# Optimization experiments

Measured on AMD Instinct MI355X. Metric: run time of the kernel, lower is better.

Reference implementation:

```python
import jax, jax.numpy as jnp
import numpy as np

B, C, L = 8, 256, 4096
OC = C // 2  # out_channels default
EPS = 1e-5


def setup_inputs() -> dict:
    key = jax.random.key(0)
    ks = jax.random.split(key, 12)
    s_in = 1.0 / np.sqrt(C)   # conv1d default init scale (kaiming-uniform-ish)
    s_oc = 1.0 / np.sqrt(OC)
    return {
        "x": jax.random.normal(ks[0], (B, C, L), dtype=jnp.float32),
        "g_w": jax.random.uniform(ks[1], (OC, C), jnp.float32, -s_in, s_in),
        "g_b": jax.random.uniform(ks[2], (OC,), jnp.float32, -s_in, s_in),
        # theta/phi weights: nn.init.normal_(w, 0.02) -> mean 0.02, std 1
        "theta_w": 0.02 + jax.random.normal(ks[3], (OC, C), dtype=jnp.float32),
        "theta_b": jax.random.uniform(ks[4], (OC,), jnp.float32, -s_in, s_in),
        "phi_w": 0.02 + jax.random.normal(ks[5], (OC, C), dtype=jnp.float32),
        "phi_b": jax.random.uniform(ks[6], (OC,), jnp.float32, -s_in, s_in),
        "W_w": jax.random.uniform(ks[7], (C, OC), jnp.float32, -s_oc, s_oc),
        "W_b": jax.random.uniform(ks[8], (C,), jnp.float32, -s_oc, s_oc),
        # BN affine: init to zero in the original; use small random for a meaningful test
        "gamma": 0.1 * jax.random.normal(ks[9], (C,), dtype=jnp.float32),
        "beta": 0.1 * jax.random.normal(ks[10], (C,), dtype=jnp.float32),
    }


def reference(x, g_w, g_b, theta_w, theta_b, phi_w, phi_b, W_w, W_b, gamma, beta):
    # x: (b, c, l). 1x1 conv == per-position linear map over channels.
    g_x = jnp.einsum('oc,bcl->bol', g_w, x) + g_b[None, :, None]        # (b, oc, l)
    theta_x = jnp.einsum('oc,bcl->bol', theta_w, x) + theta_b[None, :, None]
    phi_x = jnp.einsum('oc,bcl->bol', phi_w, x) + phi_b[None, :, None]
    # f = theta^T phi : (b, l, l) quadratic score matrix (no softmax)
    f = jnp.einsum('bok,bom->bkm', theta_x, phi_x)
    N = f.shape[-1]
    # y = (f @ g^T) / N, returned in (b, oc, l) layout
    y = jnp.einsum('bkm,bom->bok', f, g_x) / N
    W_y = jnp.einsum('co,bol->bcl', W_w, y) + W_b[None, :, None]        # (b, c, l)
    # BatchNorm1d (training mode: batch statistics over (b, l), biased var)
    mean = jnp.mean(W_y, axis=(0, 2), keepdims=True)
    var = jnp.mean((W_y - mean) ** 2, axis=(0, 2), keepdims=True)
    W_y = (W_y - mean) * jax.lax.rsqrt(var + EPS)
    W_y = gamma[None, :, None] * W_y + beta[None, :, None]
    return W_y + x  # residual
```

## Files before the change

### kernel.cpp

```cpp
#include <hip/hip_runtime.h>
#include <hip/hip_bf16.h>

#define B_ 8
#define C_ 256
#define OC_ 128
#define L_ 4096
#define EPS_ 1e-5f
#define SPLITK 8

typedef unsigned short u16;
typedef __attribute__((ext_vector_type(4))) unsigned short u16x4;
typedef __attribute__((ext_vector_type(4))) float f32x4;
typedef __attribute__((ext_vector_type(8))) short bf16x8;

__device__ inline u16 f2bf(float f) {
  union { __hip_bfloat16 h; u16 u; } v;
  v.h = __float2bfloat16(f);
  return v.u;
}
__device__ inline float bf2f(u16 u) {
  union { float f; unsigned u; } v;
  v.u = ((unsigned)u) << 16;
  return v.f;
}

__device__ inline void gload_lds16(const void* g, void* lds) {
  __builtin_amdgcn_global_load_lds(
      (const __attribute__((address_space(1))) unsigned int*)g,
      (__attribute__((address_space(3))) unsigned int*)lds, 16, 0, 0);
}

__device__ inline float blockReduceSum(float v, float* red, int nthreads) {
  int tid = threadIdx.x;
  red[tid] = v;
  __syncthreads();
  for (int s = nthreads >> 1; s > 0; s >>= 1) {
    if (tid < s) red[tid] += red[tid + s];
    __syncthreads();
  }
  float r = red[0];
  __syncthreads();
  return r;
}

__global__ __launch_bounds__(256) void k_cvt(const float* __restrict__ x,
                                             u16* __restrict__ Xb,
                                             u16* __restrict__ XbT,
                                             float* __restrict__ spartial) {
  __shared__ u16 T[64][73];
  __shared__ float P[64][17];
  const int b = blockIdx.z, c0 = blockIdx.y * 64, l0 = blockIdx.x * 64;
  const int tid = threadIdx.x;
#pragma unroll
  for (int it = 0; it < 4; ++it) {
    int idx = it * 256 + tid;
    int row = idx >> 4;
    int col = (idx & 15) << 2;
    size_t gi = ((size_t)(b * C_ + c0 + row)) * L_ + l0 + col;
    float4 v = *(const float4*)(x + gi);
    u16 u0 = f2bf(v.x), u1 = f2bf(v.y), u2 = f2bf(v.z), u3 = f2bf(v.w);
    u16x4 u = {u0, u1, u2, u3};
    *(u16x4*)(Xb + gi) = u;
    T[row][col] = u0; T[row][col + 1] = u1; T[row][col + 2] = u2; T[row][col + 3] = u3;
    P[row][idx & 15] = v.x + v.y + v.z + v.w;
  }
  __syncthreads();
  if (tid < 64) {
    float acc = 0.f;
#pragma unroll
    for (int j = 0; j < 16; j++) acc += P[tid][j];
    spartial[(size_t)(b * C_ + c0 + tid) * 64 + blockIdx.x] = acc;
  }
#pragma unroll
  for (int it = 0; it < 4; ++it) {
    int idx = it * 256 + tid;
    int lrow = idx >> 4;
    int ccol = (idx & 15) << 2;
    u16x4 u = {T[ccol][lrow], T[ccol + 1][lrow], T[ccol + 2][lrow], T[ccol + 3][lrow]};
    *(u16x4*)(XbT + ((size_t)b * L_ + l0 + lrow) * C_ + c0 + ccol) = u;
  }
}

__global__ __launch_bounds__(256) void k_xxt(const u16* __restrict__ Xb,
                                             float* __restrict__ Spart) {
  const int b = blockIdx.z, split = blockIdx.y;
  const int ti = blockIdx.x >> 1, tj = blockIdx.x & 1;
  __shared__ u16 lds[2 * 128 * 64];
  const int tid = threadIdx.x, lane = tid & 63;
  const int wid = tid >> 6, wr = wid >> 1, wc = wid & 1;
  const u16* Arows = Xb + ((size_t)b * C_ + ti * 128) * L_;
  const u16* Brows = Xb + ((size_t)b * C_ + tj * 128) * L_;
  const int k0 = split * (L_ / SPLITK);
  f32x4 acc[4][4] = {};
  for (int kt = 0; kt < L_ / SPLITK; kt += 64) {
    __syncthreads();
#pragma unroll
    for (int ch = 0; ch < 4; ch++) {
      int d = ch * 4096 + tid * 16;
      int row = d >> 7;
      int kb = (d & 127) ^ ((row & 7) << 4);
      gload_lds16(Arows + (size_t)row * L_ + k0 + kt + (kb >> 1), (char*)lds + d);
      gload_lds16(Brows + (size_t)row * L_ + k0 + kt + (kb >> 1), (char*)lds + 16384 + d);
    }
    asm volatile("s_waitcnt vmcnt(0)" ::: "memory");
    __syncthreads();
#pragma unroll
    for (int ks = 0; ks < 2; ks++) {
      bf16x8 af[4], bfr[4];
#pragma unroll
      for (int m = 0; m < 4; m++) {
        int row = wr * 64 + m * 16 + (lane & 15);
        int kb = ((ks << 6) + ((lane >> 4) << 4)) ^ ((row & 7) << 4);
        af[m] = *(const bf16x8*)((const char*)lds + row * 128 + kb);
      }
#pragma unroll
      for (int n = 0; n < 4; n++) {
        int row = wc * 64 + n * 16 + (lane & 15);
        int kb = ((ks << 6) + ((lane >> 4) << 4)) ^ ((row & 7) << 4);
        bfr[n] = *(const bf16x8*)((const char*)lds + 16384 + row * 128 + kb);
      }
#pragma unroll
      for (int m = 0; m < 4; m++)
#pragma unroll
        for (int n = 0; n < 4; n++)
          acc[m][n] = __builtin_amdgcn_mfma_f32_16x16x32_bf16(af[m], bfr[n], acc[m][n], 0, 0, 0);
    }
  }
  float* Sp = Spart + ((size_t)split * B_ + b) * C_ * C_;
#pragma unroll
  for (int m = 0; m < 4; m++)
#pragma unroll
    for (int n = 0; n < 4; n++) {
      int r0 = ti * 128 + wr * 64 + m * 16 + ((lane >> 4) << 2);
      int c0 = tj * 128 + wc * 64 + n * 16 + (lane & 15);
#pragma unroll
      for (int r = 0; r < 4; r++)
        Sp[(size_t)(r0 + r) * C_ + c0] = acc[m][n][r];
    }
}

__global__ __launch_bounds__(256) void k_sreduce(const float* __restrict__ Spart,
                                                 const float* __restrict__ spartial,
                                                 const float* __restrict__ g_w,
                                                 float* __restrict__ S,
                                                 float* __restrict__ s,
                                                 float* __restrict__ gwT) {
  const int bid = blockIdx.x, tid = threadIdx.x;
  if (bid < (B_ * C_ * C_) / 256) {
    size_t idx = (size_t)bid * 256 + tid;
    float acc = 0.f;
    for (int sp = 0; sp < SPLITK; sp++) acc += Spart[(size_t)sp * B_ * C_ * C_ + idx];
    S[idx] = acc;
  } else if (bid < (B_ * C_ * C_) / 256 + (B_ * C_) / 256) {
    int idx2 = (bid - (B_ * C_ * C_) / 256) * 256 + tid;
    const float4* sp = (const float4*)(spartial + (size_t)idx2 * 64);
    float acc = 0.f;
#pragma unroll
    for (int i = 0; i < 16; i++) { float4 v = sp[i]; acc += v.x + v.y + v.z + v.w; }
    s[idx2] = acc;
  } else {
    int t = bid - ((B_ * C_ * C_) / 256 + (B_ * C_) / 256);
    int o = t * 8 + (tid & 7);
    int cbase = (tid >> 3) * 8;
#pragma unroll
    for (int k = 0; k < 8; k++) {
      int c = cbase + k;
      gwT[c * OC_ + o] = g_w[o * C_ + c];
    }
  }
}

__global__ __launch_bounds__(256) void k_mid1(const float* __restrict__ S,
                                              const float* __restrict__ s,
                                              const float* __restrict__ phi_w,
                                              const float* __restrict__ phi_b,
                                              const float* __restrict__ gwT,
                                              const float* __restrict__ g_b,
                                              float* __restrict__ MT) {
  const int b = blockIdx.x >> 7, op = blockIdx.x & 127;
  const int tid = threadIdx.x;
  __shared__ float sl[C_], pw[C_], t2[C_], red[256];
  sl[tid] = s[b * C_ + tid];
  pw[tid] = phi_w[op * C_ + tid];
  __syncthreads();
  float ps_op = blockReduceSum(pw[tid] * sl[tid], red, 256);
  float phb = phi_b[op];
  const float* Sb = S + (size_t)b * C_ * C_;
  float t1 = 0.f;
  for (int cp = 0; cp < C_; cp++) t1 += pw[cp] * Sb[(size_t)cp * C_ + tid];
  t2[tid] = t1 + phb * sl[tid];
  __syncthreads();
  const int o = tid & 127, half = tid >> 7;
  float part = 0.f;
  for (int cc = 0; cc < 128; cc++) {
    int cidx = half * 128 + cc;
    part += t2[cidx] * gwT[cidx * OC_ + o];
  }
  red[tid] = part;
  __syncthreads();
  if (tid < OC_) {
    float val = red[tid] + red[tid + 128] + (ps_op + (float)L_ * phb) * g_b[tid];
    MT[((size_t)b * OC_ + tid) * OC_ + op] = val;
  }
}

__global__ __launch_bounds__(128) void k_mid2stats(const float* __restrict__ MT,
                                                   const float* __restrict__ W_w,
                                                   const float* __restrict__ theta_w,
                                                   const float* __restrict__ theta_b,
                                                   const float* __restrict__ W_b,
                                                   const float* __restrict__ S,
                                                   const float* __restrict__ s,
                                                   float* __restrict__ Q,
                                                   float* __restrict__ qv,
                                                   float* __restrict__ sum1,
                                                   float* __restrict__ sum2) {
  const int b = blockIdx.x >> 8, c = blockIdx.x & 255;
  const int tid = threadIdx.x;
  __shared__ float wr_[OC_], U_s[OC_], red[OC_], qrow[C_];
  wr_[tid] = W_w[c * OC_ + tid];
  __syncthreads();
  const float* MTb = MT + (size_t)b * OC_ * OC_;
  float acc = 0.f;
  for (int o = 0; o < OC_; o++) acc += wr_[o] * MTb[(size_t)o * OC_ + tid];
  acc *= (1.0f / (float)L_);
  U_s[tid] = acc;
  float tot = blockReduceSum(acc * theta_b[tid], red, OC_);
  float q_val = tot + W_b[c];
  if (tid == 0) qv[b * C_ + c] = q_val;
  float a2[2];
#pragma unroll
  for (int h = 0; h < 2; h++) {
    int ch = tid + h * OC_;
    float a = 0.f;
    for (int op = 0; op < OC_; op++) a += U_s[op] * theta_w[(size_t)op * C_ + ch];
    a2[h] = a;
    qrow[ch] = a;
    Q[((size_t)b * C_ + c) * C_ + ch] = a;
  }
  __syncthreads();
  const float* Sb = S + (size_t)b * C_ * C_;
  float rq = 0.f, qssum = 0.f;
#pragma unroll
  for (int h = 0; h < 2; h++) {
    int ch = tid + h * OC_;
    float r = 0.f;
    for (int cp = 0; cp < C_; cp++) r += qrow[cp] * Sb[(size_t)cp * C_ + ch];
    rq += r * a2[h];
    qssum += a2[h] * s[b * C_ + ch];
  }
  float e2 = blockReduceSum(rq, red, OC_);
  float qs = blockReduceSum(qssum, red, OC_);
  if (tid == 0) {
    sum1[b * C_ + c] = qs + (float)L_ * q_val;
    sum2[b * C_ + c] = e2 + 2.f * q_val * qs + (float)L_ * q_val * q_val;
  }
}

__global__ __launch_bounds__(256) void k_out(const float* __restrict__ Q,
                                             const float* __restrict__ qv,
                                             const float* __restrict__ sum1,
                                             const float* __restrict__ sum2,
                                             const float* __restrict__ gamma,
                                             const float* __restrict__ beta,
                                             const u16* __restrict__ XbT,
                                             const u16* __restrict__ Xb,
                                             float* __restrict__ out) {
  const int b = blockIdx.z, ct = blockIdx.y, lt = blockIdx.x;
  __shared__ u16 lds[128 * 64];
  __shared__ float gsc_s[128], qp_s[128];
  const int tid = threadIdx.x, lane = tid & 63;
  const int wid = tid >> 6, wr = wid >> 1, wc = wid & 1;
  if (tid < 128) {
    int c = ct * 128 + tid;
    float m = 0.f, e = 0.f;
#pragma unroll
    for (int bb = 0; bb < B_; bb++) {
      m += sum1[bb * C_ + c];
      e += sum2[bb * C_ + c];
    }
    const float inv_n = 1.f / (float)(B_ * L_);
    m *= inv_n;
    e *= inv_n;
    float var = e - m * m;
    float g = gamma[c] * rsqrtf(var + EPS_);
    gsc_s[tid] = g;
    qp_s[tid] = g * (qv[b * C_ + c] - m) + beta[c];
  }
  const u16* Bbase = XbT + ((size_t)b * L_ + lt * 128) * C_;
  const float* Abase = Q + ((size_t)b * C_ + ct * 128) * C_;
  f32x4 acc[4][4] = {};
  for (int k0 = 0; k0 < C_; k0 += 64) {
    __syncthreads();
#pragma unroll
    for (int ch = 0; ch < 4; ch++) {
      int d = ch * 4096 + tid * 16;
      int row = d >> 7;
      int kb = (d & 127) ^ ((row & 7) << 4);
      gload_lds16(Bbase + (size_t)row * C_ + k0 + (kb >> 1), (char*)lds + d);
    }
    asm volatile("s_waitcnt vmcnt(0)" ::: "memory");
    __syncthreads();
#pragma unroll
    for (int ks = 0; ks < 2; ks++) {
      bf16x8 af[4], bfr[4];
#pragma unroll
      for (int m = 0; m < 4; m++) {
        int row = wr * 64 + m * 16 + (lane & 15);
        int kk = k0 + ks * 32 + ((lane >> 4) << 3);
        float g = gsc_s[row];
        const float* src = Abase + (size_t)row * C_ + kk;
        float4 v0 = *(const float4*)src;
        float4 v1 = *(const float4*)(src + 4);
        bf16x8 a;
        a[0] = (short)f2bf(g * v0.x); a[1] = (short)f2bf(g * v0.y);
        a[2] = (short)f2bf(g * v0.z); a[3] = (short)f2bf(g * v0.w);
        a[4] = (short)f2bf(g * v1.x); a[5] = (short)f2bf(g * v1.y);
        a[6] = (short)f2bf(g * v1.z); a[7] = (short)f2bf(g * v1.w);
        af[m] = a;
      }
#pragma unroll
      for (int n = 0; n < 4; n++) {
        int row = wc * 64 + n * 16 + (lane & 15);
        int kb = ((ks << 6) + ((lane >> 4) << 4)) ^ ((row & 7) << 4);
        bfr[n] = *(const bf16x8*)((const char*)lds + row * 128 + kb);
      }
#pragma unroll
      for (int m = 0; m < 4; m++)
#pragma unroll
        for (int n = 0; n < 4; n++)
          acc[m][n] = __builtin_amdgcn_mfma_f32_16x16x32_bf16(af[m], bfr[n], acc[m][n], 0, 0, 0);
    }
  }
#pragma unroll
  for (int m = 0; m < 4; m++)
#pragma unroll
    for (int n = 0; n < 4; n++) {
      int cl = wr * 64 + m * 16 + ((lane >> 4) << 2);
      int c = ct * 128 + cl;
      int l = lt * 128 + wc * 64 + n * 16 + (lane & 15);
#pragma unroll
      for (int r = 0; r < 4; r++) {
        size_t gi = ((size_t)b * C_ + c + r) * L_ + l;
        out[gi] = acc[m][n][r] + bf2f(Xb[gi]) + qp_s[cl + r];
      }
    }
}

extern "C" void kernel_launch(void* const* d_in, const int* in_sizes, int n_in,
                              void* d_out, int out_size, void* d_ws, size_t ws_size,
                              hipStream_t stream) {
  const float* x       = (const float*)d_in[0];
  const float* g_w     = (const float*)d_in[1];
  const float* g_b     = (const float*)d_in[2];
  const float* theta_w = (const float*)d_in[3];
  const float* theta_b = (const float*)d_in[4];
  const float* phi_w   = (const float*)d_in[5];
  const float* phi_b   = (const float*)d_in[6];
  const float* W_w     = (const float*)d_in[7];
  const float* W_b     = (const float*)d_in[8];
  const float* gamma   = (const float*)d_in[9];
  const float* beta    = (const float*)d_in[10];
  float* out = (float*)d_out;

  float* ws = (float*)d_ws;
  size_t off = 0;
  float* Spart    = ws + off; off += (size_t)SPLITK * B_ * C_ * C_;
  float* S        = ws + off; off += (size_t)B_ * C_ * C_;
  float* spartial = ws + off; off += (size_t)B_ * C_ * 64;
  float* s_       = ws + off; off += B_ * C_;
  float* gwT      = ws + off; off += C_ * OC_;
  float* MT       = ws + off; off += (size_t)B_ * OC_ * OC_;
  float* qv       = ws + off; off += B_ * C_;
  float* Q        = ws + off; off += (size_t)B_ * C_ * C_;
  float* sum1     = ws + off; off += B_ * C_;
  float* sum2     = ws + off; off += B_ * C_;
  u16* Xb  = (u16*)(ws + off); off += (size_t)B_ * C_ * L_ / 2;
  u16* XbT = (u16*)(ws + off); off += (size_t)B_ * C_ * L_ / 2;

  k_cvt<<<dim3(L_ / 64, C_ / 64, B_), 256, 0, stream>>>(x, Xb, XbT, spartial);
  k_xxt<<<dim3(4, SPLITK, B_), 256, 0, stream>>>(Xb, Spart);
  k_sreduce<<<(B_ * C_ * C_) / 256 + (B_ * C_) / 256 + 16, 256, 0, stream>>>(
      Spart, spartial, g_w, S, s_, gwT);
  k_mid1<<<B_ * OC_, 256, 0, stream>>>(S, s_, phi_w, phi_b, gwT, g_b, MT);
  k_mid2stats<<<B_ * C_, 128, 0, stream>>>(MT, W_w, theta_w, theta_b, W_b, S, s_,
                                           Q, qv, sum1, sum2);
  k_out<<<dim3(L_ / 128, C_ / 128, B_), 256, 0, stream>>>(Q, qv, sum1, sum2, gamma,
                                                          beta, XbT, Xb, out);
}
```

Before: 118.4 us.

## Register-block small mid kernels to reuse S/MT loads across multiple output rows

The two small matrix-chain kernels (k_mid1, k_mid2stats) now each compute 8 or 16 output rows per block. This reuses every streamed load of S, MT, gwT and theta_w across several accumulators instead of reloading them for each row. Block reductions now use wave shuffles instead of a tree in shared memory with many barriers. The per-column partial sums are stored transposed so the reduction reads coalesced memory. Launching far fewer blocks (128 instead of 1024 or 2048) risks lower GPU occupancy and more register pressure.

```diff
diff --git a/kernel.cpp b/kernel.cpp
--- a/kernel.cpp
+++ b/kernel.cpp
@@ -28,19 +28,6 @@
   __builtin_amdgcn_global_load_lds(
       (const __attribute__((address_space(1))) unsigned int*)g,
       (__attribute__((address_space(3))) unsigned int*)lds, 16, 0, 0);
-}
-
-__device__ inline float blockReduceSum(float v, float* red, int nthreads) {
-  int tid = threadIdx.x;
-  red[tid] = v;
-  __syncthreads();
-  for (int s = nthreads >> 1; s > 0; s >>= 1) {
-    if (tid < s) red[tid] += red[tid + s];
-    __syncthreads();
-  }
-  float r = red[0];
-  __syncthreads();
-  return r;
 }
 
 __global__ __launch_bounds__(256) void k_cvt(const float* __restrict__ x,
@@ -69,7 +56,7 @@
     float acc = 0.f;
 #pragma unroll
     for (int j = 0; j < 16; j++) acc += P[tid][j];
-    spartial[(size_t)(b * C_ + c0 + tid) * 64 + blockIdx.x] = acc;
+    spartial[(size_t)blockIdx.x * (B_ * C_) + b * C_ + c0 + tid] = acc;
   }
 #pragma unroll
   for (int it = 0; it < 4; ++it) {
@@ -153,10 +140,9 @@
     S[idx] = acc;
   } else if (bid < (B_ * C_ * C_) / 256 + (B_ * C_) / 256) {
     int idx2 = (bid - (B_ * C_ * C_) / 256) * 256 + tid;
-    const float4* sp = (const float4*)(spartial + (size_t)idx2 * 64);
     float acc = 0.f;
-#pragma unroll
-    for (int i = 0; i < 16; i++) { float4 v = sp[i]; acc += v.x + v.y + v.z + v.w; }
+#pragma unroll 8
+    for (int i = 0; i < 64; i++) acc += spartial[(size_t)i * (B_ * C_) + idx2];
     s[idx2] = acc;
   } else {
     int t = bid - ((B_ * C_ * C_) / 256 + (B_ * C_) / 256);
@@ -177,83 +163,138 @@
                                               const float* __restrict__ gwT,
                                               const float* __restrict__ g_b,
                                               float* __restrict__ MT) {
-  const int b = blockIdx.x >> 7, op = blockIdx.x & 127;
+  const int b = blockIdx.x >> 4, ot = blockIdx.x & 15;
   const int tid = threadIdx.x;
-  __shared__ float sl[C_], pw[C_], t2[C_], red[256];
+  __shared__ float pw[8][257], t2[8][256], sl[256], ps_s[8], pb_s[8], redw[4][8];
   sl[tid] = s[b * C_ + tid];
-  pw[tid] = phi_w[op * C_ + tid];
-  __syncthreads();
-  float ps_op = blockReduceSum(pw[tid] * sl[tid], red, 256);
-  float phb = phi_b[op];
+#pragma unroll
+  for (int r = 0; r < 8; r++) pw[r][tid] = phi_w[(ot * 8 + r) * C_ + tid];
+  if (tid < 8) pb_s[tid] = phi_b[ot * 8 + tid];
+  __syncthreads();
+  float acc[8] = {};
   const float* Sb = S + (size_t)b * C_ * C_;
-  float t1 = 0.f;
-  for (int cp = 0; cp < C_; cp++) t1 += pw[cp] * Sb[(size_t)cp * C_ + tid];
-  t2[tid] = t1 + phb * sl[tid];
+#pragma unroll 4
+  for (int cp = 0; cp < C_; cp++) {
+    float sv = Sb[(size_t)cp * C_ + tid];
+#pragma unroll
+    for (int r = 0; r < 8; r++) acc[r] += pw[r][cp] * sv;
+  }
+  {
+    const int lane = tid & 63, w = tid >> 6;
+#pragma unroll
+    for (int r = 0; r < 8; r++) {
+      float v = pw[r][tid] * sl[tid];
+#pragma unroll
+      for (int off = 1; off < 64; off <<= 1) v += __shfl_xor(v, off, 64);
+      if (lane == 0) redw[w][r] = v;
+    }
+  }
+#pragma unroll
+  for (int r = 0; r < 8; r++) t2[r][tid] = acc[r] + pb_s[r] * sl[tid];
+  __syncthreads();
+  if (tid < 8) ps_s[tid] = redw[0][tid] + redw[1][tid] + redw[2][tid] + redw[3][tid];
   __syncthreads();
   const int o = tid & 127, half = tid >> 7;
-  float part = 0.f;
-  for (int cc = 0; cc < 128; cc++) {
-    int cidx = half * 128 + cc;
-    part += t2[cidx] * gwT[cidx * OC_ + o];
-  }
-  red[tid] = part;
-  __syncthreads();
-  if (tid < OC_) {
-    float val = red[tid] + red[tid + 128] + (ps_op + (float)L_ * phb) * g_b[tid];
-    MT[((size_t)b * OC_ + tid) * OC_ + op] = val;
-  }
-}
-
-__global__ __launch_bounds__(128) void k_mid2stats(const float* __restrict__ MT,
-                                                   const float* __restrict__ W_w,
-                                                   const float* __restrict__ theta_w,
-                                                   const float* __restrict__ theta_b,
-                                                   const float* __restrict__ W_b,
-                                                   const float* __restrict__ S,
-                                                   const float* __restrict__ s,
-                                                   float* __restrict__ Q,
-                                                   float* __restrict__ qv,
-                                                   float* __restrict__ sum1,
-                                                   float* __restrict__ sum2) {
-  const int b = blockIdx.x >> 8, c = blockIdx.x & 255;
+  float macc[4] = {};
+#pragma unroll 4
+  for (int c = 0; c < C_; c++) {
+    float gv = gwT[c * OC_ + o];
+#pragma unroll
+    for (int rr = 0; rr < 4; rr++) macc[rr] += t2[half * 4 + rr][c] * gv;
+  }
+  float gb = g_b[o];
+#pragma unroll
+  for (int rr = 0; rr < 4; rr++) {
+    int r = half * 4 + rr;
+    int op = ot * 8 + r;
+    MT[((size_t)b * OC_ + o) * OC_ + op] = macc[rr] + (ps_s[r] + (float)L_ * pb_s[r]) * gb;
+  }
+}
+
+__global__ __launch_bounds__(256) void k_mid2(const float* __restrict__ MT,
+                                              const float* __restrict__ W_w,
+                                              const float* __restrict__ theta_w,
+                                              const float* __restrict__ theta_b,
+                                              const float* __restrict__ W_b,
+                                              const float* __restrict__ S,
+                                              const float* __restrict__ s,
+                                              float* __restrict__ Q,
+                                              float* __restrict__ qv,
+                                              float* __restrict__ sum1,
+                                              float* __restrict__ sum2) {
+  const int b = blockIdx.x >> 4, ct = blockIdx.x & 15;
   const int tid = threadIdx.x;
-  __shared__ float wr_[OC_], U_s[OC_], red[OC_], qrow[C_];
-  wr_[tid] = W_w[c * OC_ + tid];
-  __syncthreads();
-  const float* MTb = MT + (size_t)b * OC_ * OC_;
-  float acc = 0.f;
-  for (int o = 0; o < OC_; o++) acc += wr_[o] * MTb[(size_t)o * OC_ + tid];
-  acc *= (1.0f / (float)L_);
-  U_s[tid] = acc;
-  float tot = blockReduceSum(acc * theta_b[tid], red, OC_);
-  float q_val = tot + W_b[c];
-  if (tid == 0) qv[b * C_ + c] = q_val;
-  float a2[2];
-#pragma unroll
-  for (int h = 0; h < 2; h++) {
-    int ch = tid + h * OC_;
+  __shared__ float ww[16][130], u_s[16][130], qtile[16][256];
+  __shared__ float tb[128], s_l[256], q_s[16], redw[2][4][16];
+  s_l[tid] = s[b * C_ + tid];
+  if (tid < 128) tb[tid] = theta_b[tid];
+#pragma unroll
+  for (int rr = 0; rr < 8; rr++) {
+    int idx = rr * 256 + tid;
+    ww[idx >> 7][idx & 127] = W_w[(ct * 16 + (idx >> 7)) * OC_ + (idx & 127)];
+  }
+  __syncthreads();
+  const int op = tid & 127, chalf = tid >> 7;
+  {
+    float uacc[8] = {};
+    const float* MTb = MT + (size_t)b * OC_ * OC_;
+#pragma unroll 4
+    for (int o = 0; o < OC_; o++) {
+      float mv = MTb[(size_t)o * OC_ + op];
+#pragma unroll
+      for (int r = 0; r < 8; r++) uacc[r] += ww[chalf * 8 + r][o] * mv;
+    }
+#pragma unroll
+    for (int r = 0; r < 8; r++) u_s[chalf * 8 + r][op] = uacc[r] * (1.f / (float)L_);
+  }
+  __syncthreads();
+  if (tid < 16) {
     float a = 0.f;
-    for (int op = 0; op < OC_; op++) a += U_s[op] * theta_w[(size_t)op * C_ + ch];
-    a2[h] = a;
-    qrow[ch] = a;
-    Q[((size_t)b * C_ + c) * C_ + ch] = a;
-  }
-  __syncthreads();
+    for (int o2 = 0; o2 < OC_; o2++) a += u_s[tid][o2] * tb[o2];
+    float qval = a + W_b[ct * 16 + tid];
+    q_s[tid] = qval;
+    qv[b * C_ + ct * 16 + tid] = qval;
+  }
+  float qacc[16] = {};
+#pragma unroll 2
+  for (int o = 0; o < OC_; o++) {
+    float tv = theta_w[(size_t)o * C_ + tid];
+#pragma unroll
+    for (int r = 0; r < 16; r++) qacc[r] += u_s[r][o] * tv;
+  }
+#pragma unroll
+  for (int r = 0; r < 16; r++) {
+    qtile[r][tid] = qacc[r];
+    Q[((size_t)b * C_ + ct * 16 + r) * C_ + tid] = qacc[r];
+  }
+  __syncthreads();
+  float yacc[16] = {};
   const float* Sb = S + (size_t)b * C_ * C_;
-  float rq = 0.f, qssum = 0.f;
-#pragma unroll
-  for (int h = 0; h < 2; h++) {
-    int ch = tid + h * OC_;
-    float r = 0.f;
-    for (int cp = 0; cp < C_; cp++) r += qrow[cp] * Sb[(size_t)cp * C_ + ch];
-    rq += r * a2[h];
-    qssum += a2[h] * s[b * C_ + ch];
-  }
-  float e2 = blockReduceSum(rq, red, OC_);
-  float qs = blockReduceSum(qssum, red, OC_);
-  if (tid == 0) {
-    sum1[b * C_ + c] = qs + (float)L_ * q_val;
-    sum2[b * C_ + c] = e2 + 2.f * q_val * qs + (float)L_ * q_val * q_val;
+#pragma unroll 4
+  for (int cp = 0; cp < C_; cp++) {
+    float sv = Sb[(size_t)cp * C_ + tid];
+#pragma unroll
+    for (int r = 0; r < 16; r++) yacc[r] += qtile[r][cp] * sv;
+  }
+  const int lane = tid & 63, w = tid >> 6;
+#pragma unroll
+  for (int r = 0; r < 16; r++) {
+    float pe = yacc[r] * qtile[r][tid];
+    float pq = qtile[r][tid] * s_l[tid];
+#pragma unroll
+    for (int off = 1; off < 64; off <<= 1) {
+      pe += __shfl_xor(pe, off, 64);
+      pq += __shfl_xor(pq, off, 64);
+    }
+    if (lane == 0) { redw[0][w][r] = pe; redw[1][w][r] = pq; }
+  }
+  __syncthreads();
+  if (tid < 16) {
+    float e2 = redw[0][0][tid] + redw[0][1][tid] + redw[0][2][tid] + redw[0][3][tid];
+    float qs = redw[1][0][tid] + redw[1][1][tid] + redw[1][2][tid] + redw[1][3][tid];
+    float qval = q_s[tid];
+    sum1[b * C_ + ct * 16 + tid] = qs + (float)L_ * qval;
+    sum2[b * C_ + ct * 16 + tid] = e2 + 2.f * qval * qs + (float)L_ * qval * qval;
   }
 }
 
@@ -382,9 +423,9 @@
   k_xxt<<<dim3(4, SPLITK, B_), 256, 0, stream>>>(Xb, Spart);
   k_sreduce<<<(B_ * C_ * C_) / 256 + (B_ * C_) / 256 + 16, 256, 0, stream>>>(
       Spart, spartial, g_w, S, s_, gwT);
-  k_mid1<<<B_ * OC_, 256, 0, stream>>>(S, s_, phi_w, phi_b, gwT, g_b, MT);
-  k_mid2stats<<<B_ * C_, 128, 0, stream>>>(MT, W_w, theta_w, theta_b, W_b, S, s_,
-                                           Q, qv, sum1, sum2);
+  k_mid1<<<B_ * 16, 256, 0, stream>>>(S, s_, phi_w, phi_b, gwT, g_b, MT);
+  k_mid2<<<B_ * 16, 256, 0, stream>>>(MT, W_w, theta_w, theta_b, W_b, S, s_,
+                                      Q, qv, sum1, sum2);
   k_out<<<dim3(L_ / 128, C_ / 128, B_), 256, 0, stream>>>(Q, qv, sum1, sum2, gamma,
                                                           beta, XbT, Xb, out);
 }
```

Measured after the change: 153.6 us. 29.7% more time.
